# Kernel optimization log

Measured on AMD Instinct MI355X. Metric: run time of the kernel, lower is better.

Reference implementation:

```python
import jax, jax.numpy as jnp
import numpy as np

B, C, T, H, K = 512, 64, 512, 128, 16
EPS_BN = 1e-5


def setup_inputs() -> dict:
    key = jax.random.key(0)
    ks = jax.random.split(key, 8)
    s = 0.05
    return {
        "x": jax.random.normal(ks[0], (B, C, T), jnp.float32),
        "conv1_w": jax.random.normal(ks[1], (H, C, 3), jnp.float32) * s,
        "conv1_b": jnp.zeros((H,), jnp.float32),
        "conv2_w": jax.random.normal(ks[2], (H, H, 3), jnp.float32) * s,
        "conv2_b": jnp.zeros((H,), jnp.float32),
        "bnt1_g": jnp.ones((H,), jnp.float32), "bnt1_b": jnp.zeros((H,), jnp.float32),
        "bnt2_g": jnp.ones((H,), jnp.float32), "bnt2_b": jnp.zeros((H,), jnp.float32),
        "W1": jax.random.normal(ks[3], (T, H), jnp.float32) * s, "b1": jnp.zeros((H,), jnp.float32),
        "g1": jnp.ones((H,), jnp.float32), "be1": jnp.zeros((H,), jnp.float32),
        "W2": jax.random.normal(ks[4], (H, H), jnp.float32) * s, "b2": jnp.zeros((H,), jnp.float32),
        "g2": jnp.ones((H,), jnp.float32), "be2": jnp.zeros((H,), jnp.float32),
        "W3": jax.random.normal(ks[5], (H, H), jnp.float32) * s, "b3": jnp.zeros((H,), jnp.float32),
        "g3": jnp.ones((H,), jnp.float32), "be3": jnp.zeros((H,), jnp.float32),
    }


def _bn_nc(z, g, b):
    # BatchNorm1d on (N, C) with batch statistics (training-mode normalization)
    m = z.mean(0)
    v = z.var(0)
    return (z - m) * jax.lax.rsqrt(v + EPS_BN) * g + b


def _bn_ncl(z, g, b):
    # BatchNorm1d on (N, C, L)
    m = z.mean((0, 2), keepdims=True)
    v = z.var((0, 2), keepdims=True)
    return (z - m) * jax.lax.rsqrt(v + EPS_BN) * g[None, :, None] + b[None, :, None]


def _conv1d(z, w, b):
    y = jax.lax.conv_general_dilated(z, w, (1,), "SAME",
                                     dimension_numbers=("NCH", "OIH", "NCH"))
    return y + b[None, :, None]


def _forward(x, conv1_w, conv1_b, conv2_w, conv2_b, bnt1_g, bnt1_b, bnt2_g, bnt2_b,
             W1, b1, g1, be1, W2, b2, g2, be2, W3, b3, g3, be3):
    # temporal branch: computed but unused in the output (faithful to the source)
    ht = jax.nn.relu(_bn_ncl(_conv1d(x, conv1_w, conv1_b), bnt1_g, bnt1_b))
    ht = jax.nn.relu(_bn_ncl(_conv1d(ht, conv2_w, conv2_b), bnt2_g, bnt2_b))

    # dynamic graph: cosine similarity averaged over batch, top-k neighbors per channel
    xn = x / jnp.maximum(jnp.linalg.norm(x, axis=2, keepdims=True), 1e-12)
    sim = jnp.einsum("bct,bdt->cd", xn, xn) / x.shape[0]  # (C, C)
    _, nbr = jax.lax.top_k(sim, K)                        # (C, K)
    src = jnp.repeat(jnp.arange(C), K)                    # (C*K,)
    dst = nbr.reshape(-1)                                 # (C*K,)
    offs = (jnp.arange(B) * C)[:, None]
    N = B * C
    sl = jnp.arange(N)
    # edge_index[0]=source node i, edge_index[1]=its top-k neighbor; plus GCN self-loops
    es = jnp.concatenate([(src[None, :] + offs).reshape(-1), sl])
    ed = jnp.concatenate([(dst[None, :] + offs).reshape(-1), sl])

    deg = jax.ops.segment_sum(jnp.ones(es.shape[0], x.dtype), ed, num_segments=N)
    dinv = jax.lax.rsqrt(deg)  # deg >= 1 due to self-loops
    enorm = dinv[es] * dinv[ed]

    def gcn(h, W, b):
        hw = h @ W
        return jax.ops.segment_sum(hw[es] * enorm[:, None], ed, num_segments=N) + b

    # source does permute(0,2,1).view(B*C, T): a flat reshape of the (B, T, C) tensor
    nodes = jnp.transpose(x, (0, 2, 1)).reshape(N, T)
    h = jax.nn.relu(_bn_nc(gcn(nodes, W1, b1), g1, be1))
    h = jax.nn.relu(_bn_nc(gcn(h, W2, b2), g2, be2))
    h = jax.nn.relu(_bn_nc(gcn(h, W3, b3), g3, be3))
    return h.reshape(B, C * H)


def reference(x, conv1_w, conv1_b, conv2_w, conv2_b, bnt1_g, bnt1_b, bnt2_g, bnt2_b,
              W1, b1, g1, be1, W2, b2, g2, be2, W3, b3, g3, be3):
    return _forward(x, conv1_w, conv1_b, conv2_w, conv2_b, bnt1_g, bnt1_b,
                    bnt2_g, bnt2_b, W1, b1, g1, be1, W2, b2, g2, be2,
                    W3, b3, g3, be3)
```

## Files before the change

kernel.cpp:

```cpp
#include <hip/hip_runtime.h>
#include <math.h>

#define B_  512
#define C_  64
#define T_  512
#define H_  128
#define N_  (B_*C_)

typedef unsigned int   uint_;
typedef unsigned short ushort_;
typedef unsigned long long ull_;

typedef __attribute__((ext_vector_type(8))) short bf8v;
typedef __attribute__((ext_vector_type(4))) float f4v;

#define OFF_SIMP   0u
#define OFF_Z2     0u
#define OFF_Z1     8388608u
#define OFF_Z3     16777216u
#define OFF_WT1    25165824u
#define OFF_WT2    25296896u
#define OFF_WT3    25329664u
#define OFF_MASKS  25362432u
#define OFF_BNPART 25406464u
#define OFF_BNP2   25930752u
#define OFF_XH     33554432u

__device__ __forceinline__ ushort_ f2bf(float f) {
    uint_ u = __float_as_uint(f);
    u = (u + 0x7FFFu + ((u >> 16) & 1u)) >> 16;
    return (ushort_)u;
}
__device__ __forceinline__ float bf2f(ushort_ s) {
    return __uint_as_float(((uint_)s) << 16);
}

__device__ __forceinline__ void gload_lds16(const void* g, void* l) {
    __builtin_amdgcn_global_load_lds(
        (const __attribute__((address_space(1))) void*)g,
        (__attribute__((address_space(3))) void*)l, 16, 0, 0);
}

__device__ __forceinline__ void m_preamble_wave0(const ull_* __restrict__ masks,
                                                 ull_* nbrmS, float* dvS, int t)
{
    if (t < 64) {
        ull_ mask = masks[t];
        nbrmS[t] = mask;
        int deg = 1;
#pragma unroll
        for (int d = 0; d < 64; ++d) {
            ull_ bal = __ballot((int)((mask >> d) & 1ull));
            if (t == d) deg += (int)__popcll(bal);
        }
        dvS[t] = 1.0f / sqrtf((float)deg);
    }
}

__device__ __forceinline__ void m_build(const ull_* nbrmS, const float* dvS,
                                        int t, uint_ m8[8])
{
    const int d = t >> 2, q = t & 3;
    const float dvd = dvS[d];
#pragma unroll
    for (int p = 0; p < 8; ++p) {
        int c0 = 16 * q + 2 * p, c1 = c0 + 1;
        float w0 = (float)((int)((nbrmS[c0] >> d) & 1ull) + (c0 == d ? 1 : 0));
        float w1 = (float)((int)((nbrmS[c1] >> d) & 1ull) + (c1 == d ? 1 : 0));
        m8[p] = (uint_)f2bf(w0 * dvS[c0] * dvd) |
                ((uint_)f2bf(w1 * dvS[c1] * dvd) << 16);
    }
}

__global__ __launch_bounds__(512, 4) void k_gramw(const float* __restrict__ x,
    float* __restrict__ simpart, ushort_* __restrict__ Xhg,
    const float* __restrict__ W1, const float* __restrict__ W2,
    const float* __restrict__ W3,
    ushort_* __restrict__ Wt1, ushort_* __restrict__ Wt2, ushort_* __restrict__ Wt3)
{
    __shared__ __align__(16) char smem[35584];
    __shared__ float  gd[64];
    __shared__ double rn[64];
    const int blk = blockIdx.x;
    const int t = threadIdx.x;

    if (blk < 512) {
        ushort_* Xh = (ushort_*)smem;
        ushort_* Xl = (ushort_*)(smem + 17408);
        const int b = blk;
        const int w = t >> 6, l = t & 63;
        const int lr = l & 15, lg = l >> 4;
        const int rp = w >> 1, ch = w & 1;

        f4v acc[2];
#pragma unroll
        for (int i = 0; i < 2; ++i) acc[i] = (f4v)0.f;

        const float* xb = x + (size_t)b * (C_ * T_);

        for (int j = 0; j < 4; ++j) {
#pragma unroll
            for (int it = 0; it < 4; ++it) {
                int i = t + 512 * it;
                int c = i >> 5, t4 = i & 31;
                float4 v = *(const float4*)&xb[(size_t)c * T_ + 128 * j + 4 * t4];
                ushort_ h0 = f2bf(v.x), h1 = f2bf(v.y), h2 = f2bf(v.z), h3 = f2bf(v.w);
                uint2 ph;
                ph.x = (uint_)h0 | ((uint_)h1 << 16);
                ph.y = (uint_)h2 | ((uint_)h3 << 16);
                float e0 = v.x - bf2f(h0), e1 = v.y - bf2f(h1);
                float e2 = v.z - bf2f(h2), e3 = v.w - bf2f(h3);
                uint2 pl;
                pl.x = (uint_)f2bf(e0) | ((uint_)f2bf(e1) << 16);
                pl.y = (uint_)f2bf(e2) | ((uint_)f2bf(e3) << 16);
                *(uint2*)&Xh[c * 136 + 4 * t4] = ph;
                *(uint2*)&Xl[c * 136 + 4 * t4] = pl;
                *(uint2*)&Xhg[(((size_t)(b * 64 + c)) << 9) + 128 * j + 4 * t4] = ph;
            }
            __syncthreads();

#pragma unroll
            for (int s = 0; s < 4; ++s) {
                bf8v ah = *(const bf8v*)&Xh[(16 * rp + lr) * 136 + 32 * s + 8 * lg];
                bf8v al = *(const bf8v*)&Xl[(16 * rp + lr) * 136 + 32 * s + 8 * lg];
#pragma unroll
                for (int i = 0; i < 2; ++i) {
                    const int ct = 2 * ch + i;
                    bf8v bh = *(const bf8v*)&Xh[(16 * ct + lr) * 136 + 32 * s + 8 * lg];
                    bf8v bl = *(const bf8v*)&Xl[(16 * ct + lr) * 136 + 32 * s + 8 * lg];
                    acc[i] = __builtin_amdgcn_mfma_f32_16x16x32_bf16(ah, bh, acc[i], 0, 0, 0);
                    acc[i] = __builtin_amdgcn_mfma_f32_16x16x32_bf16(ah, bl, acc[i], 0, 0, 0);
                    acc[i] = __builtin_amdgcn_mfma_f32_16x16x32_bf16(al, bh, acc[i], 0, 0, 0);
                }
            }
            __syncthreads();
        }

        {
            const int di = rp - 2 * ch;
            if ((di == 0 || di == 1) && lg == (lr >> 2))
                gd[16 * rp + lr] = acc[di][lr & 3];
        }
        __syncthreads();
        if (t < 64) rn[t] = 1.0 / fmax(sqrt((double)gd[t]), 1e-12);
        __syncthreads();

        float* sp = simpart + (size_t)b * 4096;
#pragma unroll
        for (int i = 0; i < 2; ++i)
#pragma unroll
            for (int reg = 0; reg < 4; ++reg) {
                int rc = 16 * rp + 4 * lg + reg;
                int cc = 16 * (2 * ch + i) + lr;
                sp[rc * 64 + cc] = (float)((double)acc[i][reg] * rn[rc] * rn[cc]);
            }
    } else {
        float* L = (float*)smem;
        const int pblk = blk - 512;
        if (pblk < 8) {
#pragma unroll
            for (int it = 0; it < 4; ++it) {
                int i = t + 512 * it;
                int ri = i >> 5, f4 = i & 31;
                int m = ri >> 3, cr = ri & 7;
                *(float4*)&L[ri * 132 + 4 * f4] =
                    *(const float4*)&W1[(size_t)(64 * m + 8 * pblk + cr) * H_ + 4 * f4];
            }
            __syncthreads();
            int f = t >> 2, q = t & 3;
            uint_ buf[8];
#pragma unroll
            for (int jj = 0; jj < 8; ++jj) {
                int k0 = 16 * q + 2 * jj;
                int c0 = k0 >> 3, m0 = k0 & 7;
                int c1 = (k0 + 1) >> 3, m1 = (k0 + 1) & 7;
                buf[jj] = (uint_)f2bf(L[(m0 * 8 + c0) * 132 + f]) |
                          ((uint_)f2bf(L[(m1 * 8 + c1) * 132 + f]) << 16);
            }
            ushort_* dst = Wt1 + (size_t)f * 512 + 64 * pblk + 16 * q;
            uint4 v0 = {buf[0], buf[1], buf[2], buf[3]};
            uint4 v1 = {buf[4], buf[5], buf[6], buf[7]};
            *(uint4*)&dst[0] = v0;
            *(uint4*)&dst[8] = v1;
        } else {
            const float* W = (pblk < 10) ? W2 : W3;
            ushort_*     O = (pblk < 10) ? Wt2 : Wt3;
            int kb = (pblk - 8) & 1;
#pragma unroll
            for (int it = 0; it < 4; ++it) {
                int i = t + 512 * it;
                int ri = i >> 5, f4 = i & 31;
                *(float4*)&L[ri * 132 + 4 * f4] =
                    *(const float4*)&W[(size_t)(64 * kb + ri) * H_ + 4 * f4];
            }
            __syncthreads();
            int f = t >> 2, q = t & 3;
            uint_ buf[8];
#pragma unroll
            for (int jj = 0; jj < 8; ++jj) {
                int k0 = 16 * q + 2 * jj;
                buf[jj] = (uint_)f2bf(L[k0 * 132 + f]) |
                          ((uint_)f2bf(L[(k0 + 1) * 132 + f]) << 16);
            }
            ushort_* dst = O + (size_t)f * 128 + 64 * kb + 16 * q;
            uint4 v0 = {buf[0], buf[1], buf[2], buf[3]};
            uint4 v1 = {buf[4], buf[5], buf[6], buf[7]};
            *(uint4*)&dst[0] = v0;
            *(uint4*)&dst[8] = v1;
        }
    }
}

__global__ __launch_bounds__(1024) void k_simrank(const float* __restrict__ simpart,
                                                  ull_* __restrict__ masks)
{
    __shared__ double part[16][64];
    __shared__ double sd[64];
    const int c = blockIdx.x;
    const int t = threadIdx.x;
    const int d = t & 63, g = t >> 6;

    double a = 0.0;
    const float* sp = simpart + (size_t)c * 64 + d;
    for (int i = 0; i < 32; ++i)
        a += (double)sp[(size_t)(g + 16 * i) * 4096];
    part[g][d] = a;
    __syncthreads();

    if (t < 64) {
        double s = 0.0;
#pragma unroll
        for (int q = 0; q < 16; ++q) s += part[q][t];
        sd[t] = s;
        int rank = 0;
#pragma unroll
        for (int dp = 0; dp < 64; ++dp) {
            double w = sd[dp];
            rank += (w > s || (w == s && dp < t)) ? 1 : 0;
        }
        ull_ m = __ballot(rank < 16);
        if (t == 0) masks[c] = m;
    }
}

__device__ __forceinline__ void mfma_epilogue(char* smem, int b, int t,
    f4v acc[8], const float* __restrict__ bias, const uint_ m8[8],
    ushort_* __restrict__ Zout, float* __restrict__ bnpart)
{
    const int l = t & 63, w = t >> 6;
    const int lr = l & 15, lg = l >> 4;

    ushort_* Yt  = (ushort_*)smem;
    ushort_* Ml  = (ushort_*)(smem + 22528);
    ushort_* Zst = (ushort_*)(smem + 33792);

#pragma unroll
    for (int nt = 0; nt < 8; ++nt) {
        uint2 p;
        p.x = (uint_)f2bf(acc[nt][0]) | ((uint_)f2bf(acc[nt][1]) << 16);
        p.y = (uint_)f2bf(acc[nt][2]) | ((uint_)f2bf(acc[nt][3]) << 16);
        *(uint2*)&Yt[(16 * nt + lr) * 88 + 16 * w + 4 * lg] = p;
    }
    {
        const int d = t >> 2, q = t & 3;
        uint4 v0 = {m8[0], m8[1], m8[2], m8[3]};
        uint4 v1 = {m8[4], m8[5], m8[6], m8[7]};
        *(uint4*)&Ml[d * 88 + 16 * q]     = v0;
        *(uint4*)&Ml[d * 88 + 16 * q + 8] = v1;
    }
    __syncthreads();

    f4v z[8];
#pragma unroll
    for (int nt = 0; nt < 8; ++nt) z[nt] = (f4v)0.f;
#pragma unroll
    for (int cs = 0; cs < 2; ++cs) {
        bf8v mf = *(const bf8v*)&Ml[(16 * w + lr) * 88 + 32 * cs + 8 * lg];
#pragma unroll
        for (int nt = 0; nt < 8; ++nt) {
            bf8v yf = *(const bf8v*)&Yt[(16 * nt + lr) * 88 + 32 * cs + 8 * lg];
            z[nt] = __builtin_amdgcn_mfma_f32_16x16x32_bf16(mf, yf, z[nt], 0, 0, 0);
        }
    }

#pragma unroll
    for (int nt = 0; nt < 8; ++nt) {
        float bv = bias[16 * nt + lr];
#pragma unroll
        for (int reg = 0; reg < 4; ++reg)
            Zst[(16 * w + 4 * lg + reg) * 136 + 16 * nt + lr] = f2bf(z[nt][reg] + bv);
    }
    __syncthreads();

    if (t < 128) {
        float s = 0.f, s2 = 0.f;
        for (int r = 0; r < 64; ++r) {
            float v = bf2f(Zst[r * 136 + t]);
            s += v; s2 += v * v;
        }
        bnpart[b * 256 + t]       = s;
        bnpart[b * 256 + 128 + t] = s2;
    }
#pragma unroll
    for (int it = 0; it < 4; ++it) {
        int i = t + 256 * it;
        int r = i >> 4, seg = i & 15;
        *(uint4*)&Zout[((size_t)(b * 64 + r)) * 128 + 8 * seg] =
            *(const uint4*)&Zst[r * 136 + 8 * seg];
    }
}

__global__ __launch_bounds__(256) void k_mgemm1(const ushort_* __restrict__ Xh,
    const ushort_* __restrict__ Wt, const float* __restrict__ bias,
    const ull_* __restrict__ masks, ushort_* __restrict__ Zout,
    float* __restrict__ bnpart)
{
    __shared__ __align__(16) char smem[51456];
    __shared__ ull_  nbrmS[64];
    __shared__ float dvS[64];
    ushort_* Al = (ushort_*)smem;
    ushort_* Wl = (ushort_*)(smem + 16384);

    const int b = blockIdx.x;
    const int t = threadIdx.x;
    const int l = t & 63, w = t >> 6;
    const int lr = l & 15, lg = l >> 4;

    m_preamble_wave0(masks, nbrmS, dvS, t);

    f4v acc[8];
#pragma unroll
    for (int nt = 0; nt < 8; ++nt) acc[nt] = (f4v)0.f;

    for (int j = 0; j < 4; ++j) {
        {
            const char* asrc = (const char*)(Xh + (((size_t)(b * 64 + 16 * j)) << 9)) + t * 16;
            char* adst = smem + t * 16;
#pragma unroll
            for (int i2 = 0; i2 < 4; ++i2)
                gload_lds16(asrc + i2 * 4096, adst + i2 * 4096);
        }
        {
            const int fr = t >> 4, seg = t & 15;
            const char* wsrc = (const char*)(Wt + (size_t)fr * 512 + 128 * j + seg * 8);
            char* wdst = smem + 16384 + t * 16;
#pragma unroll
            for (int i2 = 0; i2 < 8; ++i2)
                gload_lds16(wsrc + i2 * 16384, wdst + i2 * 4096);
        }
        __syncthreads();
#pragma unroll
        for (int s = 0; s < 4; ++s) {
            bf8v af = *(const bf8v*)&Al[(4 * s + lg) * 512 + 128 * w + 8 * lr];
#pragma unroll
            for (int nt = 0; nt < 8; ++nt) {
                bf8v bfv = *(const bf8v*)&Wl[(16 * nt + lr) * 128 + 32 * s + 8 * lg];
                acc[nt] = __builtin_amdgcn_mfma_f32_16x16x32_bf16(af, bfv, acc[nt], 0, 0, 0);
            }
        }
        __syncthreads();
    }

    uint_ m8[8];
    m_build(nbrmS, dvS, t, m8);
    mfma_epilogue(smem, b, t, acc, bias, m8, Zout, bnpart);
}

__global__ __launch_bounds__(256) void k_mgemm23(const ushort_* __restrict__ Zin,
    const double* __restrict__ bnp2, const float* __restrict__ g,
    const float* __restrict__ be, const ushort_* __restrict__ Wt,
    const float* __restrict__ bias, const ull_* __restrict__ masks,
    ushort_* __restrict__ Zout, float* __restrict__ bnpart)
{
    __shared__ __align__(16) char smem[52224];
    __shared__ float ssL[256];
    __shared__ ull_  nbrmS[64];
    __shared__ float dvS[64];
    ushort_* Al = (ushort_*)smem;
    ushort_* Wl = (ushort_*)(smem + 17408);

    const int b = blockIdx.x;
    const int t = threadIdx.x;
    const int l = t & 63, w = t >> 6;
    const int lr = l & 15, lg = l >> 4;

    {
        double* sumsL = (double*)smem;
        double a = 0.0;
        for (int q = 0; q < 32; ++q) a += bnp2[(size_t)q * 256 + t];
        sumsL[t] = a;
        m_preamble_wave0(masks, nbrmS, dvS, t);
        __syncthreads();
        if (t < 128) {
            double s = sumsL[t], s2 = sumsL[128 + t];
            double mean = s * (1.0 / 32768.0);
            double var  = s2 * (1.0 / 32768.0) - mean * mean;
            double rstd = 1.0 / sqrt(var + 1e-5);
            float sc = (float)((double)g[t] * rstd);
            ssL[t]       = sc;
            ssL[128 + t] = (float)((double)be[t] - mean * (double)sc);
        }
        __syncthreads();
    }

    {
        const char* wsrc = (const char*)Wt + t * 16;
        char* wdst = smem + 17408 + t * 16;
#pragma unroll
        for (int i2 = 0; i2 < 8; ++i2)
            gload_lds16(wsrc + i2 * 4096, wdst + i2 * 4096);
    }

    f4v acc[8];
#pragma unroll
    for (int nt = 0; nt < 8; ++nt) acc[nt] = (f4v)0.f;

#pragma unroll
    for (int it = 0; it < 4; ++it) {
        int i = t + 256 * it;
        int r = i >> 4, seg = i & 15;
        uint4 v = *(const uint4*)&Zin[((size_t)(b * 64 + r)) * 128 + 8 * seg];
        uint_ w0[4] = {v.x, v.y, v.z, v.w};
        uint_ o[4];
#pragma unroll
        for (int p = 0; p < 4; ++p) {
            int f0 = 8 * seg + 2 * p;
            float z0 = bf2f((ushort_)(w0[p] & 0xFFFF));
            float z1 = bf2f((ushort_)(w0[p] >> 16));
            float h0 = fmaxf(fmaf(z0, ssL[f0],     ssL[128 + f0]),     0.f);
            float h1 = fmaxf(fmaf(z1, ssL[f0 + 1], ssL[128 + f0 + 1]), 0.f);
            o[p] = (uint_)f2bf(h0) | ((uint_)f2bf(h1) << 16);
        }
        uint4 ov = {o[0], o[1], o[2], o[3]};
        *(uint4*)&Al[r * 136 + 8 * seg] = ov;
    }
    __syncthreads();
#pragma unroll
    for (int s = 0; s < 4; ++s) {
        bf8v af = *(const bf8v*)&Al[(16 * w + lr) * 136 + 32 * s + 8 * lg];
#pragma unroll
        for (int nt = 0; nt < 8; ++nt) {
            bf8v bfv = *(const bf8v*)&Wl[(16 * nt + lr) * 128 + 32 * s + 8 * lg];
            acc[nt] = __builtin_amdgcn_mfma_f32_16x16x32_bf16(af, bfv, acc[nt], 0, 0, 0);
        }
    }
    __syncthreads();

    uint_ m8[8];
    m_build(nbrmS, dvS, t, m8);
    mfma_epilogue(smem, b, t, acc, bias, m8, Zout, bnpart);
}

__global__ __launch_bounds__(256) void k_bnA(const float* __restrict__ bnpart,
                                             double* __restrict__ bnp2)
{
    const int t = threadIdx.x, g = blockIdx.x;
    double a = 0.0;
    for (int i = 0; i < 16; ++i)
        a += (double)bnpart[(size_t)(16 * g + i) * 256 + t];
    bnp2[(size_t)g * 256 + t] = a;
}

__global__ __launch_bounds__(256) void k_out(const ushort_* __restrict__ Z,
    const double* __restrict__ bnp2, const float* __restrict__ g,
    const float* __restrict__ be, float* __restrict__ out)
{
    __shared__ double sumsL[256];
    __shared__ float  ssL[256];
    const int b = blockIdx.x;
    const int t = threadIdx.x;

    double a = 0.0;
    for (int q = 0; q < 32; ++q) a += bnp2[(size_t)q * 256 + t];
    sumsL[t] = a;
    __syncthreads();
    if (t < 128) {
        double s = sumsL[t], s2 = sumsL[128 + t];
        double mean = s * (1.0 / 32768.0);
        double var  = s2 * (1.0 / 32768.0) - mean * mean;
        double rstd = 1.0 / sqrt(var + 1e-5);
        float sc = (float)((double)g[t] * rstd);
        ssL[t]       = sc;
        ssL[128 + t] = (float)((double)be[t] - mean * (double)sc);
    }
    __syncthreads();

    const size_t base = (size_t)b * 64 * 128;
#pragma unroll
    for (int it = 0; it < 8; ++it) {
        int i = t + 256 * it;
        int r = i >> 5, s = i & 31;
        uint2 v = *(const uint2*)&Z[base + (size_t)r * 128 + 4 * s];
        float4 sc = *(const float4*)&ssL[4 * s];
        float4 sh = *(const float4*)&ssL[128 + 4 * s];
        float z0 = bf2f((ushort_)(v.x & 0xFFFF));
        float z1 = bf2f((ushort_)(v.x >> 16));
        float z2 = bf2f((ushort_)(v.y & 0xFFFF));
        float z3 = bf2f((ushort_)(v.y >> 16));
        float4 o;
        o.x = fmaxf(fmaf(z0, sc.x, sh.x), 0.f);
        o.y = fmaxf(fmaf(z1, sc.y, sh.y), 0.f);
        o.z = fmaxf(fmaf(z2, sc.z, sh.z), 0.f);
        o.w = fmaxf(fmaf(z3, sc.w, sh.w), 0.f);
        *(float4*)&out[base + (size_t)r * 128 + 4 * s] = o;
    }
}

extern "C" void kernel_launch(void* const* d_in, const int* in_sizes, int n_in,
                              void* d_out, int out_size, void* d_ws, size_t ws_size,
                              hipStream_t stream)
{
    (void)in_sizes; (void)n_in; (void)out_size; (void)ws_size;

    const float* x   = (const float*)d_in[0];
    const float* W1  = (const float*)d_in[9];
    const float* b1  = (const float*)d_in[10];
    const float* g1  = (const float*)d_in[11];
    const float* be1 = (const float*)d_in[12];
    const float* W2  = (const float*)d_in[13];
    const float* b2  = (const float*)d_in[14];
    const float* g2  = (const float*)d_in[15];
    const float* be2 = (const float*)d_in[16];
    const float* W3  = (const float*)d_in[17];
    const float* b3  = (const float*)d_in[18];
    const float* g3  = (const float*)d_in[19];
    const float* be3 = (const float*)d_in[20];

    char* ws = (char*)d_ws;
    float*   simp   = (float*)(ws + OFF_SIMP);
    ull_*    masks  = (ull_*)(ws + OFF_MASKS);
    ushort_* Wt1    = (ushort_*)(ws + OFF_WT1);
    ushort_* Wt2    = (ushort_*)(ws + OFF_WT2);
    ushort_* Wt3    = (ushort_*)(ws + OFF_WT3);
    float*   bnpart = (float*)(ws + OFF_BNPART);
    double*  bnp2   = (double*)(ws + OFF_BNP2);
    ushort_* Xh     = (ushort_*)(ws + OFF_XH);
    ushort_* Z1     = (ushort_*)(ws + OFF_Z1);
    ushort_* Z2     = (ushort_*)(ws + OFF_Z2);
    ushort_* Z3     = (ushort_*)(ws + OFF_Z3);
    float*   out    = (float*)d_out;

    k_gramw<<<dim3(524), dim3(512), 0, stream>>>(x, simp, Xh, W1, W2, W3, Wt1, Wt2, Wt3);
    k_simrank<<<dim3(64), dim3(1024), 0, stream>>>(simp, masks);

    k_mgemm1<<<dim3(512), dim3(256), 0, stream>>>(Xh, Wt1, b1, masks, Z1, bnpart);
    k_bnA<<<dim3(32), dim3(256), 0, stream>>>(bnpart, bnp2);

    k_mgemm23<<<dim3(512), dim3(256), 0, stream>>>(Z1, bnp2, g1, be1, Wt2, b2, masks, Z2, bnpart);
    k_bnA<<<dim3(32), dim3(256), 0, stream>>>(bnpart, bnp2);

    k_mgemm23<<<dim3(512), dim3(256), 0, stream>>>(Z2, bnp2, g2, be2, Wt3, b3, masks, Z3, bnpart);
    k_bnA<<<dim3(32), dim3(256), 0, stream>>>(bnpart, bnp2);

    k_out<<<dim3(512), dim3(256), 0, stream>>>(Z3, bnp2, g3, be3, out);
}
```

Baseline: 96.22 us.

## Replace BN partial-sum reduction kernels with fixed-point global atomics

Each GEMM block now atomically adds its per-channel sum and sum-of-squares into 64-bit fixed-point accumulators, instead of writing partials that a separate k_bnA kernel reduces. This removes three small reduction launches and the 32-way partial reads in consumer kernels, at the cost of one memset and contended atomics (512 blocks onto 256 addresses). Fixed-point scaling keeps the result deterministic, though the scale factor limits precision and range.

```diff
diff --git a/kernel.cpp b/kernel.cpp
--- a/kernel.cpp
+++ b/kernel.cpp
@@ -13,6 +13,8 @@
 
 typedef __attribute__((ext_vector_type(8))) short bf8v;
 typedef __attribute__((ext_vector_type(4))) float f4v;
+
+#define BN_SCALE 4194304.0
 
 #define OFF_SIMP   0u
 #define OFF_Z2     0u
@@ -22,8 +24,7 @@
 #define OFF_WT2    25296896u
 #define OFF_WT3    25329664u
 #define OFF_MASKS  25362432u
-#define OFF_BNPART 25406464u
-#define OFF_BNP2   25930752u
+#define OFF_BNACC  25406464u
 #define OFF_XH     33554432u
 
 __device__ __forceinline__ ushort_ f2bf(float f) {
@@ -245,7 +246,7 @@
 
 __device__ __forceinline__ void mfma_epilogue(char* smem, int b, int t,
     f4v acc[8], const float* __restrict__ bias, const uint_ m8[8],
-    ushort_* __restrict__ Zout, float* __restrict__ bnpart)
+    ushort_* __restrict__ Zout, ull_* __restrict__ bnacc)
 {
     const int l = t & 63, w = t >> 6;
     const int lr = l & 15, lg = l >> 4;
@@ -298,8 +299,8 @@
             float v = bf2f(Zst[r * 136 + t]);
             s += v; s2 += v * v;
         }
-        bnpart[b * 256 + t]       = s;
-        bnpart[b * 256 + 128 + t] = s2;
+        atomicAdd(&bnacc[t],       (ull_)(long long)__double2ll_rn((double)s  * BN_SCALE));
+        atomicAdd(&bnacc[128 + t], (ull_)(long long)__double2ll_rn((double)s2 * BN_SCALE));
     }
 #pragma unroll
     for (int it = 0; it < 4; ++it) {
@@ -313,7 +314,7 @@
 __global__ __launch_bounds__(256) void k_mgemm1(const ushort_* __restrict__ Xh,
     const ushort_* __restrict__ Wt, const float* __restrict__ bias,
     const ull_* __restrict__ masks, ushort_* __restrict__ Zout,
-    float* __restrict__ bnpart)
+    ull_* __restrict__ bnacc)
 {
     __shared__ __align__(16) char smem[51456];
     __shared__ ull_  nbrmS[64];
@@ -363,14 +364,14 @@
 
     uint_ m8[8];
     m_build(nbrmS, dvS, t, m8);
-    mfma_epilogue(smem, b, t, acc, bias, m8, Zout, bnpart);
+    mfma_epilogue(smem, b, t, acc, bias, m8, Zout, bnacc);
 }
 
 __global__ __launch_bounds__(256) void k_mgemm23(const ushort_* __restrict__ Zin,
-    const double* __restrict__ bnp2, const float* __restrict__ g,
+    const ull_* __restrict__ bnaccIn, const float* __restrict__ g,
     const float* __restrict__ be, const ushort_* __restrict__ Wt,
     const float* __restrict__ bias, const ull_* __restrict__ masks,
-    ushort_* __restrict__ Zout, float* __restrict__ bnpart)
+    ushort_* __restrict__ Zout, ull_* __restrict__ bnaccOut)
 {
     __shared__ __align__(16) char smem[52224];
     __shared__ float ssL[256];
@@ -386,9 +387,7 @@
 
     {
         double* sumsL = (double*)smem;
-        double a = 0.0;
-        for (int q = 0; q < 32; ++q) a += bnp2[(size_t)q * 256 + t];
-        sumsL[t] = a;
+        sumsL[t] = (double)(long long)bnaccIn[t] * (1.0 / BN_SCALE);
         m_preamble_wave0(masks, nbrmS, dvS, t);
         __syncthreads();
         if (t < 128) {
@@ -448,21 +447,11 @@
 
     uint_ m8[8];
     m_build(nbrmS, dvS, t, m8);
-    mfma_epilogue(smem, b, t, acc, bias, m8, Zout, bnpart);
-}
-
-__global__ __launch_bounds__(256) void k_bnA(const float* __restrict__ bnpart,
-                                             double* __restrict__ bnp2)
-{
-    const int t = threadIdx.x, g = blockIdx.x;
-    double a = 0.0;
-    for (int i = 0; i < 16; ++i)
-        a += (double)bnpart[(size_t)(16 * g + i) * 256 + t];
-    bnp2[(size_t)g * 256 + t] = a;
+    mfma_epilogue(smem, b, t, acc, bias, m8, Zout, bnaccOut);
 }
 
 __global__ __launch_bounds__(256) void k_out(const ushort_* __restrict__ Z,
-    const double* __restrict__ bnp2, const float* __restrict__ g,
+    const ull_* __restrict__ bnaccIn, const float* __restrict__ g,
     const float* __restrict__ be, float* __restrict__ out)
 {
     __shared__ double sumsL[256];
@@ -470,9 +459,7 @@
     const int b = blockIdx.x;
     const int t = threadIdx.x;
 
-    double a = 0.0;
-    for (int q = 0; q < 32; ++q) a += bnp2[(size_t)q * 256 + t];
-    sumsL[t] = a;
+    sumsL[t] = (double)(long long)bnaccIn[t] * (1.0 / BN_SCALE);
     __syncthreads();
     if (t < 128) {
         double s = sumsL[t], s2 = sumsL[128 + t];
@@ -532,25 +519,22 @@
     ushort_* Wt1    = (ushort_*)(ws + OFF_WT1);
     ushort_* Wt2    = (ushort_*)(ws + OFF_WT2);
     ushort_* Wt3    = (ushort_*)(ws + OFF_WT3);
-    float*   bnpart = (float*)(ws + OFF_BNPART);
-    double*  bnp2   = (double*)(ws + OFF_BNP2);
+    ull_*    bnacc1 = (ull_*)(ws + OFF_BNACC);
+    ull_*    bnacc2 = bnacc1 + 256;
+    ull_*    bnacc3 = bnacc1 + 512;
     ushort_* Xh     = (ushort_*)(ws + OFF_XH);
     ushort_* Z1     = (ushort_*)(ws + OFF_Z1);
     ushort_* Z2     = (ushort_*)(ws + OFF_Z2);
     ushort_* Z3     = (ushort_*)(ws + OFF_Z3);
     float*   out    = (float*)d_out;
 
+    hipMemsetAsync(ws + OFF_BNACC, 0, 3 * 256 * sizeof(ull_), stream);
+
     k_gramw<<<dim3(524), dim3(512), 0, stream>>>(x, simp, Xh, W1, W2, W3, Wt1, Wt2, Wt3);
     k_simrank<<<dim3(64), dim3(1024), 0, stream>>>(simp, masks);
 
-    k_mgemm1<<<dim3(512), dim3(256), 0, stream>>>(Xh, Wt1, b1, masks, Z1, bnpart);
-    k_bnA<<<dim3(32), dim3(256), 0, stream>>>(bnpart, bnp2);
-
-    k_mgemm23<<<dim3(512), dim3(256), 0, stream>>>(Z1, bnp2, g1, be1, Wt2, b2, masks, Z2, bnpart);
-    k_bnA<<<dim3(32), dim3(256), 0, stream>>>(bnpart, bnp2);
-
-    k_mgemm23<<<dim3(512), dim3(256), 0, stream>>>(Z2, bnp2, g2, be2, Wt3, b3, masks, Z3, bnpart);
-    k_bnA<<<dim3(32), dim3(256), 0, stream>>>(bnpart, bnp2);
-
-    k_out<<<dim3(512), dim3(256), 0, stream>>>(Z3, bnp2, g3, be3, out);
-}
+    k_mgemm1<<<dim3(512), dim3(256), 0, stream>>>(Xh, Wt1, b1, masks, Z1, bnacc1);
+    k_mgemm23<<<dim3(512), dim3(256), 0, stream>>>(Z1, bnacc1, g1, be1, Wt2, b2, masks, Z2, bnacc2);
+    k_mgemm23<<<dim3(512), dim3(256), 0, stream>>>(Z2, bnacc2, g2, be2, Wt3, b3, masks, Z3, bnacc3);
+    k_out<<<dim3(512), dim3(256), 0, stream>>>(Z3, bnacc3, g3, be3, out);
+}
```

New measurement: 119.6 us. +24.3%, slower.
